# Kernel optimization log

Measured on AMD Instinct MI355X. Metric: run time of the kernel, lower is better.

Reference implementation:

```python
import jax, jax.numpy as jnp
import numpy as np

N_HEAD = 16

def _split_heads(t, n_head):
    B, S, D = t.shape
    return t.reshape(B, S, n_head, D // n_head).transpose(0, 2, 1, 3)  # [B,H,S,dh]

def setup_inputs() -> dict:
    key = jax.random.key(0)
    ks = jax.random.split(key, 12)
    nx = 1024
    B, S, Nv, Nt = 8, 1024, 49, 14
    std = 0.02
    return {
        "x": jax.random.normal(ks[0], (B, S, nx), jnp.float32),
        "visual_features": jax.random.normal(ks[1], (B, Nv, 1024), jnp.float32),
        "tags_embeddings": jax.random.normal(ks[2], (B, Nt, 400), jnp.float32),
        "W_attn": jax.random.normal(ks[3], (nx, 3 * nx), jnp.float32) * std,
        "b_attn": jnp.zeros((3 * nx,), jnp.float32),
        "W_vis": jax.random.normal(ks[4], (1024, 2 * nx), jnp.float32) * std,
        "b_vis": jnp.zeros((2 * nx,), jnp.float32),
        "W_tags": jax.random.normal(ks[5], (400, 2 * nx), jnp.float32) * std,
        "b_tags": jnp.zeros((2 * nx,), jnp.float32),
        "W_proj": jax.random.normal(ks[6], (nx, nx), jnp.float32) * std,
        "b_proj": jnp.zeros((nx,), jnp.float32),
    }

def _forward(x, visual_features, tags_embeddings, W_attn, b_attn, W_vis, b_vis,
             W_tags, b_tags, W_proj, b_proj):
    B, S, nx = x.shape
    H = N_HEAD
    dh = nx // H

    qkv = x @ W_attn + b_attn                       # [B,S,3nx]
    q, k, v = jnp.split(qkv, 3, axis=2)
    q = _split_heads(q, H)                          # [B,H,S,dh]
    k = _split_heads(k, H)
    v = _split_heads(v, H)

    # concat_features(visual): extra keys/values PREPENDED to key/value
    vis = visual_features @ W_vis + b_vis           # [B,Nv,2nx]
    vk, vv = jnp.split(vis, 2, axis=2)
    k = jnp.concatenate([_split_heads(vk, H), k], axis=-2)
    v = jnp.concatenate([_split_heads(vv, H), v], axis=-2)

    # concat_features(tags): prepended in front of [visual, text]
    tg = tags_embeddings @ W_tags + b_tags          # [B,Nt,2nx]
    tk, tv = jnp.split(tg, 2, axis=2)
    k = jnp.concatenate([_split_heads(tk, H), k], axis=-2)
    v = jnp.concatenate([_split_heads(tv, H), v], axis=-2)

    present = jnp.stack([k, v], axis=1)             # [B,2,H,ns,dh]

    nd = S
    ns = k.shape[-2]
    w = jnp.einsum('bhqd,bhkd->bhqk', q, k) / jnp.sqrt(jnp.float32(dh))
    # causal mask counting from lower-right corner: prefix (vis+tags) fully visible
    i = jnp.arange(nd)[:, None]
    j = jnp.arange(ns)[None, :]
    b = (i >= j - ns + nd).astype(w.dtype)          # [nd,ns]
    w = w * b - 10000.0 * (1.0 - b)
    w = jax.nn.softmax(w, axis=-1)

    a = jnp.einsum('bhqk,bhkd->bhqd', w, v)         # [B,H,S,dh]
    a = a.transpose(0, 2, 1, 3).reshape(B, S, nx)   # merge heads
    a = a @ W_proj + b_proj
    return a, present

def reference(x, visual_features, tags_embeddings, W_attn, b_attn, W_vis, b_vis,
              W_tags, b_tags, W_proj, b_proj):
    return _forward(x, visual_features, tags_embeddings, W_attn, b_attn,
                    W_vis, b_vis, W_tags, b_tags, W_proj, b_proj)
```

## Files before the change

kernel.cpp:

```cpp
#include <hip/hip_runtime.h>


typedef __bf16 bf16x8 __attribute__((ext_vector_type(8)));
typedef unsigned short us8 __attribute__((ext_vector_type(8)));
typedef float f32x4 __attribute__((ext_vector_type(4)));

#define NS 1087
#define NSP 1088
#define PFX 63
#define NH 16
#define DH 64
#define SEQ 1024
#define BATCH 8
#define QSCALE 0.18033688011112042f

__device__ __forceinline__ unsigned short f2bf(float f) {
  unsigned int u = __float_as_uint(f);
  u += 0x7fffu + ((u >> 16) & 1u);
  return (unsigned short)(u >> 16);
}

__device__ __forceinline__ us8 cvt8(float4 a, float4 b) {
  us8 r;
  r[0] = f2bf(a.x); r[1] = f2bf(a.y); r[2] = f2bf(a.z); r[3] = f2bf(a.w);
  r[4] = f2bf(b.x); r[5] = f2bf(b.y); r[6] = f2bf(b.z); r[7] = f2bf(b.w);
  return r;
}

__device__ __forceinline__ f32x4 mfma16(us8 a, us8 b, f32x4 c) {
  return __builtin_amdgcn_mfma_f32_16x16x32_bf16(
      __builtin_bit_cast(bf16x8, a), __builtin_bit_cast(bf16x8, b), c, 0, 0, 0);
}

__device__ __forceinline__ void gl2lds16(const void* g, void* l) {
  __builtin_amdgcn_global_load_lds(
      (__attribute__((address_space(1))) void*)(g),
      (__attribute__((address_space(3))) void*)(l), 16, 0, 0);
}

__global__ __launch_bounds__(1024) void prep_k(
    const float* __restrict__ x, unsigned short* __restrict__ x16,
    const float* __restrict__ W_attn, unsigned short* __restrict__ wat16,
    const float* __restrict__ W_proj, unsigned short* __restrict__ wpt16) {
  __shared__ float tile[32][33];
  const int bid = blockIdx.x, t = threadIdx.x;
  const int tx = t & 31, ty = t >> 5;

  if (bid < 1024) {
    const int i = bid * 1024 + t;
    const float4* p = (const float4*)x + (size_t)i * 2;
    *(us8*)(x16 + (size_t)i * 8) = cvt8(p[0], p[1]);
  } else if (bid < 4096) {
    const int b2 = bid - 1024;
    const int n0 = (b2 % 96) * 32, k0 = (b2 / 96) * 32;
    tile[ty][tx] = W_attn[(size_t)(k0 + ty) * 3072 + n0 + tx];
    __syncthreads();
    wat16[(size_t)(n0 + ty) * 1024 + k0 + tx] = f2bf(tile[tx][ty]);
  } else {
    const int b2 = bid - 4096;
    const int n0 = (b2 & 31) * 32, k0 = (b2 >> 5) * 32;
    tile[ty][tx] = W_proj[(size_t)(k0 + ty) * 1024 + n0 + tx];
    __syncthreads();
    wpt16[(size_t)(n0 + ty) * 1024 + k0 + tx] = f2bf(tile[tx][ty]);
  }
}

__global__ __launch_bounds__(256) void vtrans_k(
    const float* __restrict__ present, unsigned short* __restrict__ v16t) {
  __shared__ float tile[64][68];
  const int bh = blockIdx.y;
  const int b = bh >> 4, h = bh & 15;
  const int p0 = blockIdx.x * 64;
  const int t = threadIdx.x;
  const float* src = present + (((size_t)(b * 2 + 1) * NH + h) * NS) * DH;

  const int rr = t >> 2, c0 = (t & 3) * 16;
  const int pos = p0 + rr;
  if (pos < NS) {
    const float4* sp = (const float4*)(src + (size_t)pos * DH + c0);
#pragma unroll
    for (int j = 0; j < 4; ++j) *(float4*)&tile[rr][c0 + 4 * j] = sp[j];
  } else {
    const float4 z = {0.f, 0.f, 0.f, 0.f};
#pragma unroll
    for (int j = 0; j < 4; ++j) *(float4*)&tile[rr][c0 + 4 * j] = z;
  }
  __syncthreads();

  const int d = t >> 2, q0 = (t & 3) * 16;
  us8 o0, o1;
#pragma unroll
  for (int j = 0; j < 8; ++j) {
    o0[j] = f2bf(tile[q0 + j][d]);
    o1[j] = f2bf(tile[q0 + 8 + j][d]);
  }
  unsigned short* dst = v16t + ((size_t)bh * DH + d) * NSP + p0 + q0;
  *(us8*)dst = o0;
  *(us8*)(dst + 8) = o1;
}

template <int MODE>
__global__ __launch_bounds__(256) void gemm128(
    const unsigned short* __restrict__ A, const unsigned short* __restrict__ Bt,
    const float* __restrict__ bias, float* __restrict__ outf,
    float* __restrict__ present, unsigned short* __restrict__ q16,
    unsigned short* __restrict__ k16,
    int M, int N, int K, int nbx) {
  __shared__ unsigned short As[2][128 * 32];
  __shared__ unsigned short Bs[2][128 * 32];

  const int bid = blockIdx.x, chunk = gridDim.x >> 3;
  const int wg = (bid & 7) * chunk + (bid >> 3);
  const int bx = wg % nbx, by = wg / nbx;

  const int t = threadIdx.x, w = t >> 6, l = t & 63;
  const int lr = l & 15, lq = l >> 4;
  const int m0 = by * 128, n0 = bx * 128;
  const int wr = (w >> 1) * 64, wc = (w & 1) * 64;

  f32x4 acc[4][4] = {};

  const int arow = w * 32 + (l >> 2);
  const int acol = ((l & 3) ^ ((l >> 3) & 3)) * 8;
  const unsigned short* gA = A + (size_t)(m0 + arow) * K + acol;
  const unsigned short* gB = Bt + (size_t)(n0 + arow) * K + acol;
  const int lo = (w * 32) * 32;

  const int nk = K >> 5;
  {
    gl2lds16(gA, &As[0][lo]);
    gl2lds16(gA + (size_t)16 * K, &As[0][lo + 16 * 32]);
    gl2lds16(gB, &Bs[0][lo]);
    gl2lds16(gB + (size_t)16 * K, &Bs[0][lo + 16 * 32]);
  }

  const int csw = ((lr >> 1) & 3) * 8;
  int cur = 0;
  for (int kt = 0; kt < nk; ++kt) {
    asm volatile("s_waitcnt vmcnt(0)\n\ts_barrier" ::: "memory");
    __builtin_amdgcn_sched_barrier(0);

    if (kt + 1 < nk) {
      const size_t ko = (size_t)(kt + 1) * 32;
      const int nb = cur ^ 1;
      gl2lds16(gA + ko, &As[nb][lo]);
      gl2lds16(gA + (size_t)16 * K + ko, &As[nb][lo + 16 * 32]);
      gl2lds16(gB + ko, &Bs[nb][lo]);
      gl2lds16(gB + (size_t)16 * K + ko, &Bs[nb][lo + 16 * 32]);
    }

    us8 af[4], bfr[4];
#pragma unroll
    for (int i = 0; i < 4; ++i)
      af[i] = *(us8*)&As[cur][(wr + i * 16 + lr) * 32 + ((lq * 8) ^ csw)];
#pragma unroll
    for (int j = 0; j < 4; ++j)
      bfr[j] = *(us8*)&Bs[cur][(wc + j * 16 + lr) * 32 + ((lq * 8) ^ csw)];
#pragma unroll
    for (int i = 0; i < 4; ++i)
#pragma unroll
      for (int j = 0; j < 4; ++j)
        acc[i][j] = mfma16(af[i], bfr[j], acc[i][j]);
    cur ^= 1;
  }

#pragma unroll
  for (int i = 0; i < 4; ++i) {
    const int row0 = m0 + wr + i * 16 + lq * 4;
#pragma unroll
    for (int j = 0; j < 4; ++j) {
      const int col = n0 + wc + j * 16 + lr;
      const float bv = bias[col];
#pragma unroll
      for (int r = 0; r < 4; ++r) {
        const float v = acc[i][j][r] + bv;
        const int rr = row0 + r;
        if (MODE == 0) {
          outf[(size_t)rr * N + col] = v;
        } else {
          const int b = rr >> 10, s = rr & 1023;
          const int sec = col >> 10, cc = col & 1023, h = cc >> 6, d = cc & 63;
          const int bh = b * NH + h;
          if (sec == 0) {
            q16[((size_t)bh * SEQ + s) * DH + d] = f2bf(v * QSCALE);
          } else {
            const int pos = PFX + s;
            present[(((size_t)(b * 2 + (sec - 1)) * NH + h) * NS + pos) * DH + d] = v;
            if (sec == 1)
              k16[((size_t)bh * NSP + pos) * DH + d] = f2bf(v);
          }
        }
      }
    }
  }
}

__global__ __launch_bounds__(256) void gemm64_pfx(
    const float* __restrict__ vis, const float* __restrict__ W_vis,
    const float* __restrict__ b_vis, const float* __restrict__ tags,
    const float* __restrict__ W_tags, const float* __restrict__ b_tags,
    float* __restrict__ present, unsigned short* __restrict__ k16) {
  __shared__ __align__(16) unsigned short As[64][40];
  __shared__ __align__(16) unsigned short Bs[64][40];

  const int by = blockIdx.y;
  const bool isv = by < 7;
  const float* A = isv ? vis : tags;
  const float* W = isv ? W_vis : W_tags;
  const float* bias = isv ? b_vis : b_tags;
  const int m0 = (isv ? by : by - 7) * 64;
  const int M = isv ? 392 : 112;
  const int K = isv ? 1024 : 400;
  const int RPB = isv ? 49 : 14;
  const int POFF = isv ? 14 : 0;
  const int N = 2048;

  const int t = threadIdx.x;
  const int n0 = blockIdx.x * 64;
  const int wave = t >> 6, lane = t & 63, lr = lane & 15, lq = lane >> 4;
  const int wr = (wave >> 1) * 32, wc = (wave & 1) * 32;

  f32x4 acc00 = {0,0,0,0}, acc01 = {0,0,0,0}, acc10 = {0,0,0,0}, acc11 = {0,0,0,0};

  const int am = m0 + (t >> 2);
  const int aksub = (t & 3) * 8;
  const int bksub = t >> 3;
  const int bn = n0 + (t & 7) * 8;
  const int nk = (K + 31) / 32;

  for (int kt = 0; kt < nk; ++kt) {
    const int k0 = kt * 32;
    float4 a0 = {0,0,0,0}, a1 = {0,0,0,0};
    const int ak = k0 + aksub;
    if (am < M && ak < K) {
      const float4* ap = (const float4*)(A + (size_t)am * K + ak);
      a0 = ap[0]; a1 = ap[1];
    }
    float4 b0 = {0,0,0,0}, b1 = {0,0,0,0};
    const int bk = k0 + bksub;
    if (bk < K) {
      const float4* bp = (const float4*)(W + (size_t)bk * N + bn);
      b0 = bp[0]; b1 = bp[1];
    }
    __syncthreads();
    *(us8*)&As[t >> 2][aksub] = cvt8(a0, a1);
    {
      unsigned short tmp[8] = {f2bf(b0.x), f2bf(b0.y), f2bf(b0.z), f2bf(b0.w),
                               f2bf(b1.x), f2bf(b1.y), f2bf(b1.z), f2bf(b1.w)};
      const int nn = (t & 7) * 8;
#pragma unroll
      for (int j = 0; j < 8; ++j) Bs[nn + j][bksub] = tmp[j];
    }
    __syncthreads();

    us8 af0 = *(us8*)&As[wr + lr][lq * 8];
    us8 af1 = *(us8*)&As[wr + 16 + lr][lq * 8];
    us8 bf0 = *(us8*)&Bs[wc + lr][lq * 8];
    us8 bf1 = *(us8*)&Bs[wc + 16 + lr][lq * 8];
    acc00 = mfma16(af0, bf0, acc00);
    acc01 = mfma16(af0, bf1, acc01);
    acc10 = mfma16(af1, bf0, acc10);
    acc11 = mfma16(af1, bf1, acc11);
  }

  auto store_one = [&](float v, int row, int col) {
    if (row >= M) return;
    v += bias[col];
    const int b = row / RPB, i = row - b * RPB;
    const int sec = col >> 10, cc = col & 1023, h = cc >> 6, d = cc & 63;
    const int pos = POFF + i;
    present[(((size_t)(b * 2 + sec) * NH + h) * NS + pos) * DH + d] = v;
    if (sec == 0)
      k16[((size_t)(b * NH + h) * NSP + pos) * DH + d] = f2bf(v);
  };

#pragma unroll
  for (int r = 0; r < 4; ++r) {
    const int rbase = m0 + wr + lq * 4 + r;
    const int cbase = n0 + wc + lr;
    store_one(acc00[r], rbase,      cbase);
    store_one(acc01[r], rbase,      cbase + 16);
    store_one(acc10[r], rbase + 16, cbase);
    store_one(acc11[r], rbase + 16, cbase + 16);
  }
}

__global__ __launch_bounds__(256) void attn_kernel(
    const unsigned short* __restrict__ q16, const unsigned short* __restrict__ k16,
    const unsigned short* __restrict__ v16t, unsigned short* __restrict__ a16) {
  __shared__ unsigned short Ks[2][64 * 64];
  __shared__ unsigned short Vt[2][64 * 64];
  __shared__ unsigned short Pb[4][16][64];

  const int pair = blockIdx.x >> 7, bh = blockIdx.x & 127;
  const int b = bh >> 4, h = bh & 15;
  const int t = threadIdx.x, w = t >> 6, l = t & 63;
  const int lr = l & 15, lq = l >> 4;

  const unsigned short* Kg = k16 + (size_t)bh * NSP * DH;
  const unsigned short* Vg = v16t + (size_t)bh * DH * NSP;

  const int rsub = l >> 3;
  const int perm = ((l & 7) ^ rsub) << 3;
  const int wrow = w * 16 + rsub;
  const int swr = (lr & 7) << 3;
  int cur = 0;

  for (int seg = 0; seg < 2; ++seg) {
    const int qt = seg ? (15 - pair) : pair;
    const int q0w = qt * 64 + w * 16;

    const unsigned short* qp = q16 + ((size_t)bh * SEQ + q0w + lr) * DH;
    const us8 qa0 = *(const us8*)(qp + lq * 8);
    const us8 qa1 = *(const us8*)(qp + 32 + lq * 8);

    f32x4 o[4] = {};
    float lrow[4] = {0.f, 0.f, 0.f, 0.f};

    gl2lds16(Kg + (size_t)wrow * DH + perm,        Ks[cur] + (w * 16) * 64);
    gl2lds16(Kg + (size_t)(wrow + 8) * DH + perm,  Ks[cur] + (w * 16 + 8) * 64);
    gl2lds16(Vg + (size_t)wrow * NSP + perm,       Vt[cur] + (w * 16) * 64);
    gl2lds16(Vg + (size_t)(wrow + 8) * NSP + perm, Vt[cur] + (w * 16 + 8) * 64);

    const int ntiles = qt + 2;

    for (int kt = 0; kt < ntiles; ++kt) {
      asm volatile("s_waitcnt vmcnt(0)\n\ts_barrier" ::: "memory");
      __builtin_amdgcn_sched_barrier(0);

      if (kt + 1 < ntiles) {
        const int kp1 = (kt + 1) * 64;
        unsigned short* KsN = Ks[cur ^ 1];
        unsigned short* VtN = Vt[cur ^ 1];
        gl2lds16(Kg + (size_t)(kp1 + wrow) * DH + perm,       KsN + (w * 16) * 64);
        gl2lds16(Kg + (size_t)(kp1 + wrow + 8) * DH + perm,   KsN + (w * 16 + 8) * 64);
        gl2lds16(Vg + (size_t)wrow * NSP + kp1 + perm,        VtN + (w * 16) * 64);
        gl2lds16(Vg + (size_t)(wrow + 8) * NSP + kp1 + perm,  VtN + (w * 16 + 8) * 64);
      }

      const unsigned short* KsC = Ks[cur];
      const unsigned short* VtC = Vt[cur];

      f32x4 s[4];
      __builtin_amdgcn_s_setprio(1);
#pragma unroll
      for (int j = 0; j < 4; ++j) {
        const int ro = (j * 16 + lr) * 64;
        const us8 kb0 = *(const us8*)&KsC[ro + ((lq * 8) ^ swr)];
        const us8 kb1 = *(const us8*)&KsC[ro + ((32 + lq * 8) ^ swr)];
        f32x4 z = {};
        z = mfma16(qa0, kb0, z);
        z = mfma16(qa1, kb1, z);
        s[j] = z;
      }
      __builtin_amdgcn_s_setprio(0);

      if (kt == ntiles - 1) {
        const int kp0 = kt * 64;
#pragma unroll
        for (int r = 0; r < 4; ++r) {
          const int lim = q0w + lq * 4 + r + PFX - kp0;
#pragma unroll
          for (int j = 0; j < 4; ++j)
            if (j * 16 + lr > lim) s[j][r] = -1e30f;
        }
      }

#pragma unroll
      for (int r = 0; r < 4; ++r) {
        float p[4];
#pragma unroll
        for (int j = 0; j < 4; ++j) { p[j] = exp2f(s[j][r]); lrow[r] += p[j]; }
        const int prow = lq * 4 + r;
        const int psw = (prow & 7) << 3;
        unsigned short* pb = &Pb[w][prow][0];
#pragma unroll
        for (int j = 0; j < 4; ++j) pb[(j * 16 + lr) ^ psw] = f2bf(p[j]);
      }

      const us8 pf0 = *(const us8*)&Pb[w][lr][(lq * 8) ^ swr];
      const us8 pf1 = *(const us8*)&Pb[w][lr][(32 + lq * 8) ^ swr];
      __builtin_amdgcn_s_setprio(1);
#pragma unroll
      for (int jd = 0; jd < 4; ++jd) {
        const int ro = (jd * 16 + lr) * 64;
        const us8 vb0 = *(const us8*)&VtC[ro + ((lq * 8) ^ swr)];
        const us8 vb1 = *(const us8*)&VtC[ro + ((32 + lq * 8) ^ swr)];
        o[jd] = mfma16(pf0, vb0, o[jd]);
        o[jd] = mfma16(pf1, vb1, o[jd]);
      }
      __builtin_amdgcn_s_setprio(0);
      cur ^= 1;
    }

#pragma unroll
    for (int r = 0; r < 4; ++r) {
      float rs = lrow[r];
      rs += __shfl_xor(rs, 1);
      rs += __shfl_xor(rs, 2);
      rs += __shfl_xor(rs, 4);
      rs += __shfl_xor(rs, 8);
      const float inv = 1.0f / rs;
      const int sr = q0w + lq * 4 + r;
      unsigned short* op = a16 + ((size_t)b * SEQ + sr) * 1024 + h * DH;
#pragma unroll
      for (int jd = 0; jd < 4; ++jd) op[jd * 16 + lr] = f2bf(o[jd][r] * inv);
    }
  }
}

extern "C" void kernel_launch(void* const* d_in, const int* in_sizes, int n_in,
                              void* d_out, int out_size, void* d_ws, size_t ws_size,
                              hipStream_t stream) {
  const float* x      = (const float*)d_in[0];
  const float* vis    = (const float*)d_in[1];
  const float* tags   = (const float*)d_in[2];
  const float* W_attn = (const float*)d_in[3];
  const float* b_attn = (const float*)d_in[4];
  const float* W_vis  = (const float*)d_in[5];
  const float* b_vis  = (const float*)d_in[6];
  const float* W_tags = (const float*)d_in[7];
  const float* b_tags = (const float*)d_in[8];
  const float* W_proj = (const float*)d_in[9];
  const float* b_proj = (const float*)d_in[10];

  float* out_a   = (float*)d_out;
  float* present = out_a + (size_t)BATCH * SEQ * 1024;

  unsigned short* q16 = (unsigned short*)d_out;
  unsigned short* x16 = q16 + (size_t)8192 * 1024;

  char* ws = (char*)d_ws;
  unsigned short* a16   = (unsigned short*)ws;
  unsigned short* wat16 = (unsigned short*)(ws + 16777216);
  unsigned short* wpt16 = (unsigned short*)(ws + 23068672);
  unsigned short* k16   = (unsigned short*)(ws + 25165824);
  unsigned short* v16t  = (unsigned short*)(ws + 42991616);

  const dim3 blk(256);
  prep_k<<<dim3(5120), dim3(1024), 0, stream>>>(x, x16, W_attn, wat16, W_proj, wpt16);
  gemm128<1><<<dim3(1536), blk, 0, stream>>>(
      x16, wat16, b_attn, nullptr, present, q16, k16, 8192, 3072, 1024, 24);
  gemm64_pfx<<<dim3(32, 9), blk, 0, stream>>>(
      vis, W_vis, b_vis, tags, W_tags, b_tags, present, k16);
  vtrans_k<<<dim3(17, 128), blk, 0, stream>>>(present, v16t);
  attn_kernel<<<dim3(BATCH * NH * 8), blk, 0, stream>>>(q16, k16, v16t, a16);
  gemm128<0><<<dim3(512), blk, 0, stream>>>(
      a16, wpt16, b_proj, out_a, nullptr, nullptr, nullptr, 8192, 1024, 1024, 8);
}
```

Before: 358.0 us.

## Enlarge GEMM tiles to 256x128 with K=64 split-phase staging

Replaces the 128x128, K=32 GEMM with a 512-thread 256x128 tile and a 64-wide K step. Each K step is split into two halves so half of the next tile's loads are issued while the current half is computed, with partial vmcnt waits and an XOR swizzle over 8 chunks. It also raises MFMA wave priority with s_setprio. The aim is fewer, larger blocks with more reuse per global load and better overlap of loads and MFMAs, at the cost of more LDS (96KB per block) and extra barriers per iteration.

```diff
diff --git a/kernel.cpp b/kernel.cpp
--- a/kernel.cpp
+++ b/kernel.cpp
@@ -100,14 +100,14 @@
 }
 
 template <int MODE>
-__global__ __launch_bounds__(256) void gemm128(
+__global__ __launch_bounds__(512, 2) void gemm256(
     const unsigned short* __restrict__ A, const unsigned short* __restrict__ Bt,
     const float* __restrict__ bias, float* __restrict__ outf,
     float* __restrict__ present, unsigned short* __restrict__ q16,
     unsigned short* __restrict__ k16,
     int M, int N, int K, int nbx) {
-  __shared__ unsigned short As[2][128 * 32];
-  __shared__ unsigned short Bs[2][128 * 32];
+  __shared__ unsigned short As[2][256 * 64];
+  __shared__ unsigned short Bs[2][128 * 64];
 
   const int bid = blockIdx.x, chunk = gridDim.x >> 3;
   const int wg = (bid & 7) * chunk + (bid >> 3);
@@ -115,52 +115,85 @@
 
   const int t = threadIdx.x, w = t >> 6, l = t & 63;
   const int lr = l & 15, lq = l >> 4;
-  const int m0 = by * 128, n0 = bx * 128;
+  const int m0 = by * 256, n0 = bx * 128;
   const int wr = (w >> 1) * 64, wc = (w & 1) * 64;
 
   f32x4 acc[4][4] = {};
 
-  const int arow = w * 32 + (l >> 2);
-  const int acol = ((l & 3) ^ ((l >> 3) & 3)) * 8;
-  const unsigned short* gA = A + (size_t)(m0 + arow) * K + acol;
-  const unsigned short* gB = Bt + (size_t)(n0 + arow) * K + acol;
-  const int lo = (w * 32) * 32;
-
-  const int nk = K >> 5;
-  {
-    gl2lds16(gA, &As[0][lo]);
-    gl2lds16(gA + (size_t)16 * K, &As[0][lo + 16 * 32]);
-    gl2lds16(gB, &Bs[0][lo]);
-    gl2lds16(gB + (size_t)16 * K, &Bs[0][lo + 16 * 32]);
-  }
-
-  const int csw = ((lr >> 1) & 3) * 8;
+  const int perm = ((l & 7) ^ ((l >> 3) & 7)) << 3;
+  const unsigned short* gA = A + (size_t)(m0 + w * 32 + (l >> 3)) * K + perm;
+  const unsigned short* gB = Bt + (size_t)(n0 + w * 16 + (l >> 3)) * K + perm;
+
+  const int nk = K >> 6;
+
+  auto stage = [&](int nb, int part, size_t ko) {
+    if (part == 0) {
+      gl2lds16(gA + ko,                &As[nb][(w * 32 + 0) * 64]);
+      gl2lds16(gA + ko + (size_t)8 * K, &As[nb][(w * 32 + 8) * 64]);
+      gl2lds16(gB + ko,                &Bs[nb][(w * 16 + 0) * 64]);
+    } else {
+      gl2lds16(gA + ko + (size_t)16 * K, &As[nb][(w * 32 + 16) * 64]);
+      gl2lds16(gA + ko + (size_t)24 * K, &As[nb][(w * 32 + 24) * 64]);
+      gl2lds16(gB + ko + (size_t)8 * K,  &Bs[nb][(w * 16 + 8) * 64]);
+    }
+  };
+
+  stage(0, 0, 0);
+  stage(0, 1, 0);
+
+  const int rsw = lr & 7;
   int cur = 0;
   for (int kt = 0; kt < nk; ++kt) {
-    asm volatile("s_waitcnt vmcnt(0)\n\ts_barrier" ::: "memory");
+    const int nb = cur ^ 1;
+    const size_t ko = (size_t)(kt + 1) * 64;
+    const bool more = (kt + 1 < nk);
+
+    if (more) {
+      stage(nb, 0, ko);
+      asm volatile("s_waitcnt vmcnt(3)\n\ts_barrier" ::: "memory");
+    } else {
+      asm volatile("s_waitcnt vmcnt(0)\n\ts_barrier" ::: "memory");
+    }
     __builtin_amdgcn_sched_barrier(0);
-
-    if (kt + 1 < nk) {
-      const size_t ko = (size_t)(kt + 1) * 32;
-      const int nb = cur ^ 1;
-      gl2lds16(gA + ko, &As[nb][lo]);
-      gl2lds16(gA + (size_t)16 * K + ko, &As[nb][lo + 16 * 32]);
-      gl2lds16(gB + ko, &Bs[nb][lo]);
-      gl2lds16(gB + (size_t)16 * K + ko, &Bs[nb][lo + 16 * 32]);
-    }
-
-    us8 af[4], bfr[4];
-#pragma unroll
-    for (int i = 0; i < 4; ++i)
-      af[i] = *(us8*)&As[cur][(wr + i * 16 + lr) * 32 + ((lq * 8) ^ csw)];
-#pragma unroll
-    for (int j = 0; j < 4; ++j)
-      bfr[j] = *(us8*)&Bs[cur][(wc + j * 16 + lr) * 32 + ((lq * 8) ^ csw)];
-#pragma unroll
-    for (int i = 0; i < 4; ++i)
+    {
+      us8 af[4], bf[4];
+#pragma unroll
+      for (int i = 0; i < 4; ++i)
+        af[i] = *(const us8*)&As[cur][(wr + i * 16 + lr) * 64 + (((lq) ^ rsw) << 3)];
 #pragma unroll
       for (int j = 0; j < 4; ++j)
-        acc[i][j] = mfma16(af[i], bfr[j], acc[i][j]);
+        bf[j] = *(const us8*)&Bs[cur][(wc + j * 16 + lr) * 64 + (((lq) ^ rsw) << 3)];
+      __builtin_amdgcn_s_setprio(1);
+#pragma unroll
+      for (int i = 0; i < 4; ++i)
+#pragma unroll
+        for (int j = 0; j < 4; ++j)
+          acc[i][j] = mfma16(af[i], bf[j], acc[i][j]);
+      __builtin_amdgcn_s_setprio(0);
+    }
+    asm volatile("s_barrier" ::: "memory");
+    __builtin_amdgcn_sched_barrier(0);
+
+    if (more) stage(nb, 1, ko);
+    {
+      us8 af[4], bf[4];
+#pragma unroll
+      for (int i = 0; i < 4; ++i)
+        af[i] = *(const us8*)&As[cur][(wr + i * 16 + lr) * 64 + (((4 + lq) ^ rsw) << 3)];
+#pragma unroll
+      for (int j = 0; j < 4; ++j)
+        bf[j] = *(const us8*)&Bs[cur][(wc + j * 16 + lr) * 64 + (((4 + lq) ^ rsw) << 3)];
+      __builtin_amdgcn_s_setprio(1);
+#pragma unroll
+      for (int i = 0; i < 4; ++i)
+#pragma unroll
+        for (int j = 0; j < 4; ++j)
+          acc[i][j] = mfma16(af[i], bf[j], acc[i][j]);
+      __builtin_amdgcn_s_setprio(0);
+    }
+    asm volatile("s_barrier" ::: "memory");
+    __builtin_amdgcn_sched_barrier(0);
+
     cur ^= 1;
   }
 
@@ -439,12 +472,12 @@
 
   const dim3 blk(256);
   prep_k<<<dim3(5120), dim3(1024), 0, stream>>>(x, x16, W_attn, wat16, W_proj, wpt16);
-  gemm128<1><<<dim3(1536), blk, 0, stream>>>(
+  gemm256<1><<<dim3(768), dim3(512), 0, stream>>>(
       x16, wat16, b_attn, nullptr, present, q16, k16, 8192, 3072, 1024, 24);
   gemm64_pfx<<<dim3(32, 9), blk, 0, stream>>>(
       vis, W_vis, b_vis, tags, W_tags, b_tags, present, k16);
   vtrans_k<<<dim3(17, 128), blk, 0, stream>>>(present, v16t);
   attn_kernel<<<dim3(BATCH * NH * 8), blk, 0, stream>>>(q16, k16, v16t, a16);
-  gemm128<0><<<dim3(512), blk, 0, stream>>>(
+  gemm256<0><<<dim3(256), dim3(512), 0, stream>>>(
       a16, wpt16, b_proj, out_a, nullptr, nullptr, nullptr, 8192, 1024, 1024, 8);
 }
```

Result: slower. 384.8 us (+7.5%).
